# Kernel tuning notes

Measured on AMD Instinct MI355X. Metric: run time of the kernel, lower is better.

Reference implementation:

```python
import jax, jax.numpy as jnp
import numpy as np

WINDOW = 11
SIGMA = 1.5
CHANNELS = 3
C1 = 0.01 ** 2
C2 = 0.03 ** 2


def _gaussian_kernel(size=WINDOW, sigma=SIGMA, channels=CHANNELS):
    coords = jnp.arange(size, dtype=jnp.float32) - size // 2
    g = jnp.exp(-coords ** 2 / (2.0 * sigma ** 2))
    g = jnp.outer(g, g)
    g = g / g.sum()
    # depthwise kernel: [C, 1, K, K] (OIHW with feature_group_count=C)
    return jnp.broadcast_to(g[None, None], (channels, 1, size, size))


def _dwconv(x, kernel):
    # x: [N, C, H, W]; SAME padding, depthwise (groups = C)
    pad = WINDOW // 2
    return jax.lax.conv_general_dilated(
        x, kernel,
        window_strides=(1, 1),
        padding=[(pad, pad), (pad, pad)],
        dimension_numbers=('NCHW', 'OIHW', 'NCHW'),
        feature_group_count=CHANNELS,
    )


def setup_inputs() -> dict:
    key = jax.random.key(0)
    k1, k2 = jax.random.split(key)
    shape = (16, 3, 512, 512)
    pred = jax.random.uniform(k1, shape, dtype=jnp.float32)
    target = jax.random.uniform(k2, shape, dtype=jnp.float32)
    return {"pred": pred, "target": target}


def reference(pred, target):
    kernel = _gaussian_kernel().astype(pred.dtype)
    mu_p = _dwconv(pred, kernel)
    mu_t = _dwconv(target, kernel)
    mu_p2 = mu_p * mu_p
    mu_t2 = mu_t * mu_t
    mu_pt = mu_p * mu_t
    sigma_p2 = _dwconv(pred * pred, kernel) - mu_p2
    sigma_t2 = _dwconv(target * target, kernel) - mu_t2
    sigma_pt = _dwconv(pred * target, kernel) - mu_pt
    ssim_map = ((2.0 * mu_pt + C1) * (2.0 * sigma_pt + C2)) / (
        (mu_p2 + mu_t2 + C1) * (sigma_p2 + sigma_t2 + C2)
    )
    return 1.0 - ssim_map.mean()
```

## Files before the change

### kernel.cpp

```cpp
#include <hip/hip_runtime.h>
#include <math.h>

#define IMG_H 512
#define IMG_W 512
#define NSLOT 64
#define HT_R  56

typedef _Float16 f16x4 __attribute__((ext_vector_type(4)));
typedef _Float16 f16x8 __attribute__((ext_vector_type(8)));
typedef float    f32x4 __attribute__((ext_vector_type(4)));

__device__ __forceinline__ f16x8 pack8(const float4& a, const float4& b) {
    return f16x8{(_Float16)a.x, (_Float16)a.y, (_Float16)a.z, (_Float16)a.w,
                 (_Float16)b.x, (_Float16)b.y, (_Float16)b.z, (_Float16)b.w};
}

__device__ __forceinline__ f16x8 build_frag(int which, int l)
{
    const int lln = l & 15, llg = l >> 4;
    f16x8 f;
    #pragma unroll
    for (int j = 0; j < 8; ++j) {
        int idx = llg * 8 + j - lln - (which ? 0 : 3);
        float d = (float)(idx - 5);
        float v = 0.26601173f * exp2f(-d * d * 0.32059889f);
        f[j] = (_Float16)(((unsigned)idx <= 10u) ? v : 0.0f);
    }
    return f;
}

__global__ void ssim_frag_init(f16x8* __restrict__ frags)
{
    const int tid = threadIdx.x;
    if (tid < 128) frags[tid] = build_frag(tid >> 6, tid & 63);
}

__global__ __launch_bounds__(256, 6)
void ssim_main(const float* __restrict__ pred, const float* __restrict__ targ,
               const f16x8* __restrict__ frags, float* __restrict__ partial,
               double* __restrict__ acc, int mode)
{
    __shared__ _Float16 hT[2][5][16][HT_R];

    const int tid  = threadIdx.x;
    const int lane = tid & 63, wave = tid >> 6;
    const int ln   = lane & 15, lg = lane >> 4;
    const int ct   = wave >> 1, par = wave & 1;

    const int tx = blockIdx.x, ty = blockIdx.y, img = blockIdx.z;
    const float* __restrict__ p = pred + (size_t)img * (IMG_H * IMG_W);
    const float* __restrict__ t = targ + (size_t)img * (IMG_H * IMG_W);

    f16x8 Bw, A2w;
    if (frags) { Bw = frags[lane]; A2w = frags[64 + lane]; }
    else       { Bw = build_frag(0, lane); A2w = build_frag(1, lane); }

    const int rb0 = par ? 16 : 0;
    const int gc  = tx * 32 + ct * 16 + lg * 8 - 8;
    const bool colOK = (gc >= 0) && (gc <= IMG_W - 8);
    float4 P[2][2] = {}, T[2][2] = {};
    #pragma unroll
    for (int pos = 0; pos < 2; ++pos) {
        const int gr = ty * 32 - 5 + rb0 + 16 * pos + ln;
        if (colOK && gr >= 0 && gr < IMG_H) {
            const float* bp = p + (size_t)gr * IMG_W + gc;
            const float* bt = t + (size_t)gr * IMG_W + gc;
            P[pos][0] = ((const float4*)bp)[0];  P[pos][1] = ((const float4*)bp)[1];
            T[pos][0] = ((const float4*)bt)[0];  T[pos][1] = ((const float4*)bt)[1];
        }
    }
    const f32x4 z = {0.f, 0.f, 0.f, 0.f};

    #pragma unroll
    for (int pos = 0; pos < 2; ++pos) {
        const int rowbase = rb0 + 16 * pos;
        f16x8 pa = pack8(P[pos][0], P[pos][1]);
        f16x8 ta = pack8(T[pos][0], T[pos][1]);
        f16x8 fq[5];
        fq[0] = pa; fq[1] = ta;
        fq[2] = pa * pa; fq[3] = ta * ta; fq[4] = pa * ta;
        const int orow = rowbase + lg * 4;
        #pragma unroll
        for (int q = 0; q < 5; ++q) {
            f32x4 d = __builtin_amdgcn_mfma_f32_16x16x32_f16(fq[q], Bw, z, 0, 0, 0);
            *(f16x4*)&hT[ct][q][ln][orow] =
                f16x4{(_Float16)d[0], (_Float16)d[1], (_Float16)d[2], (_Float16)d[3]};
        }
    }

    float lsum = 0.f;
    {
        const int rbase = par * 16 + lg * 8;
        f32x4 accq[5];
        #pragma unroll
        for (int q = 0; q < 5; ++q) {
            f16x8 b = *(const f16x8*)&hT[ct][q][ln][rbase];
            accq[q] = __builtin_amdgcn_mfma_f32_16x16x32_f16(A2w, b, z, 0, 0, 0);
        }
        const float C1 = 1e-4f, C2 = 9e-4f;
        #pragma unroll
        for (int r = 0; r < 4; ++r) {
            float mp = accq[0][r], mt = accq[1][r];
            float vp = accq[2][r] - mp * mp;
            float vt = accq[3][r] - mt * mt;
            float cv = accq[4][r] - mp * mt;
            float num = (2.f * mp * mt + C1) * (2.f * cv + C2);
            float den = (mp * mp + mt * mt + C1) * (vp + vt + C2);
            lsum = fmaf(num, __builtin_amdgcn_rcpf(den), lsum);
        }
    }

    #pragma unroll
    for (int off = 32; off > 0; off >>= 1)
        lsum += __shfl_down(lsum, off, 64);
    if (lane == 0) {
        const int bid = (blockIdx.z * gridDim.y + blockIdx.y) * gridDim.x + blockIdx.x;
        if (mode == 0) partial[bid * 4 + wave] = lsum;
        else atomicAdd(&acc[(bid * 4 + wave) & (NSLOT - 1)], (double)lsum);
    }
}

__global__ void ssim_init(double* acc)
{
    if (threadIdx.x < NSLOT) acc[threadIdx.x] = 0.0;
}

__global__ __launch_bounds__(1024)
void ssim_fin_slots(const float* __restrict__ partial, float* __restrict__ out,
                    int n4, double inv_n)
{
    __shared__ double red[16];
    double s = 0.0;
    const int tid = threadIdx.x;
    for (int i = tid; i < n4; i += 1024) {
        float4 v = ((const float4*)partial)[i];
        s += (double)v.x + (double)v.y + (double)v.z + (double)v.w;
    }
    #pragma unroll
    for (int off = 32; off > 0; off >>= 1)
        s += __shfl_down(s, off, 64);
    if ((tid & 63) == 0) red[tid >> 6] = s;
    __syncthreads();
    if (tid == 0) {
        double tot = 0.0;
        #pragma unroll
        for (int w = 0; w < 16; ++w) tot += red[w];
        out[0] = (float)(1.0 - tot * inv_n);
    }
}

__global__ void ssim_fin_atomic(const double* __restrict__ acc, float* __restrict__ out,
                                double inv_n)
{
    if (threadIdx.x == 0) {
        double s = 0.0;
        for (int i = 0; i < NSLOT; ++i) s += acc[i];
        out[0] = (float)(1.0 - s * inv_n);
    }
}

extern "C" void kernel_launch(void* const* d_in, const int* in_sizes, int n_in,
                              void* d_out, int out_size, void* d_ws, size_t ws_size,
                              hipStream_t stream)
{
    const float* pred = (const float*)d_in[0];
    const float* targ = (const float*)d_in[1];
    float* out = (float*)d_out;

    const long long total = (long long)in_sizes[0];
    const int n_img = (int)(total / (IMG_H * IMG_W));
    dim3 grid(IMG_W / 32, IMG_H / 32, n_img);
    const int nblk = grid.x * grid.y * grid.z;
    const int nslots = nblk * 4;
    const double inv_n = 1.0 / (double)total;
    const size_t fragBytes = 128 * sizeof(f16x8);

    if (ws_size >= fragBytes + (size_t)nslots * sizeof(float)) {
        f16x8* frags   = (f16x8*)d_ws;
        float* partial = (float*)((char*)d_ws + fragBytes);
        hipLaunchKernelGGL(ssim_frag_init, dim3(1), dim3(128), 0, stream, frags);
        hipLaunchKernelGGL(ssim_main, grid, dim3(256), 0, stream,
                           pred, targ, (const f16x8*)frags, partial, (double*)nullptr, 0);
        hipLaunchKernelGGL(ssim_fin_slots, dim3(1), dim3(1024), 0, stream,
                           partial, out, nslots / 4, inv_n);
    } else {
        double* acc = (double*)d_ws;
        hipLaunchKernelGGL(ssim_init, dim3(1), dim3(64), 0, stream, acc);
        hipLaunchKernelGGL(ssim_main, grid, dim3(256), 0, stream,
                           pred, targ, (const f16x8*)nullptr, (float*)nullptr, acc, 1);
        hipLaunchKernelGGL(ssim_fin_atomic, dim3(1), dim3(1), 0, stream,
                           acc, out, inv_n);
    }
}
```

Before: 156.9 us.

## Fuse SSIM into one kernel with LDS-staged tiles and cross-image prefetch

Replaces the three-kernel pipeline (fragment init, main, final reduce) with a single fused kernel. Each block loads a 42x48 halo tile of pred and target into LDS once, so waves no longer refetch overlapping halo rows and columns, and it processes four images per block while prefetching the next image into registers. The final reduction uses a per-block double atomic plus a last-block counter, which removes the separate finish launch at the cost of a memset, atomic contention, and fewer blocks with more LDS barriers.

Result: slower. 262.8 us (+67.5%).

```diff
diff --git a/kernel.cpp b/kernel.cpp
--- a/kernel.cpp
+++ b/kernel.cpp
@@ -3,12 +3,20 @@
 
 #define IMG_H 512
 #define IMG_W 512
-#define NSLOT 64
-#define HT_R  56
+#define IPB   4
+#define SAB_S 56
+#define HT_S  56
 
 typedef _Float16 f16x4 __attribute__((ext_vector_type(4)));
 typedef _Float16 f16x8 __attribute__((ext_vector_type(8)));
 typedef float    f32x4 __attribute__((ext_vector_type(4)));
+
+__device__ __forceinline__ void lds_barrier() {
+    __asm__ volatile("" ::: "memory");
+    __builtin_amdgcn_s_waitcnt(0xC07F);
+    __builtin_amdgcn_s_barrier();
+    __asm__ volatile("" ::: "memory");
+}
 
 __device__ __forceinline__ f16x8 pack8(const float4& a, const float4& b) {
     return f16x8{(_Float16)a.x, (_Float16)a.y, (_Float16)a.z, (_Float16)a.w,
@@ -29,133 +37,151 @@
     return f;
 }
 
-__global__ void ssim_frag_init(f16x8* __restrict__ frags)
+__global__ __launch_bounds__(256, 4)
+void ssim_fused(const float* __restrict__ pred, const float* __restrict__ targ,
+                float* __restrict__ out, double* __restrict__ acc,
+                unsigned* __restrict__ counter, int n_img, int nblk, double inv_n)
 {
-    const int tid = threadIdx.x;
-    if (tid < 128) frags[tid] = build_frag(tid >> 6, tid & 63);
-}
-
-__global__ __launch_bounds__(256, 6)
-void ssim_main(const float* __restrict__ pred, const float* __restrict__ targ,
-               const f16x8* __restrict__ frags, float* __restrict__ partial,
-               double* __restrict__ acc, int mode)
-{
-    __shared__ _Float16 hT[2][5][16][HT_R];
+    __shared__ _Float16 sAB[2][48][SAB_S];
+    __shared__ _Float16 hT[5][32][HT_S];
+    __shared__ float red[4];
 
     const int tid  = threadIdx.x;
     const int lane = tid & 63, wave = tid >> 6;
     const int ln   = lane & 15, lg = lane >> 4;
-    const int ct   = wave >> 1, par = wave & 1;
-
-    const int tx = blockIdx.x, ty = blockIdx.y, img = blockIdx.z;
-    const float* __restrict__ p = pred + (size_t)img * (IMG_H * IMG_W);
-    const float* __restrict__ t = targ + (size_t)img * (IMG_H * IMG_W);
-
-    f16x8 Bw, A2w;
-    if (frags) { Bw = frags[lane]; A2w = frags[64 + lane]; }
-    else       { Bw = build_frag(0, lane); A2w = build_frag(1, lane); }
-
-    const int rb0 = par ? 16 : 0;
-    const int gc  = tx * 32 + ct * 16 + lg * 8 - 8;
-    const bool colOK = (gc >= 0) && (gc <= IMG_W - 8);
-    float4 P[2][2] = {}, T[2][2] = {};
+    const int tx = blockIdx.x, ty = blockIdx.y;
+
+    const int r0 = tid / 6,        g0 = tid % 6;
+    const bool has1 = (tid < 32);
+    const int r1 = (tid + 256) / 6, g1 = (tid + 256) % 6;
+
+    const int gr0 = ty * 32 - 5;
+    const int wo  = tx * 32 - 8;
+    auto valid = [&](int r, int g) {
+        int gr = gr0 + r;
+        return gr >= 0 && gr < IMG_H &&
+               !(tx == 0 && g == 0) && !(tx == 15 && g == 5);
+    };
+    const bool v0 = valid(r0, g0);
+    const bool v1 = has1 && valid(r1, g1);
+    const size_t off0 = (size_t)(gr0 + r0) * IMG_W + (wo + 8 * g0);
+    const size_t off1 = (size_t)(gr0 + r1) * IMG_W + (wo + 8 * g1);
+
+    const f16x8 Bw  = build_frag(0, lane);
+    const f16x8 A2w = build_frag(1, lane);
+    const f32x4 z = {0.f, 0.f, 0.f, 0.f};
+
+    const int imgBase = blockIdx.z * IPB;
+    float lsum = 0.f;
+
+    float4 P0a{0,0,0,0}, P0b{0,0,0,0}, T0a{0,0,0,0}, T0b{0,0,0,0};
+    float4 P1a{0,0,0,0}, P1b{0,0,0,0}, T1a{0,0,0,0}, T1b{0,0,0,0};
+    if (imgBase < n_img) {
+        const size_t ib = (size_t)imgBase * (IMG_H * IMG_W);
+        if (v0) {
+            const float* bp = pred + ib + off0; const float* bt = targ + ib + off0;
+            P0a = ((const float4*)bp)[0]; P0b = ((const float4*)bp)[1];
+            T0a = ((const float4*)bt)[0]; T0b = ((const float4*)bt)[1];
+        }
+        if (v1) {
+            const float* bp = pred + ib + off1; const float* bt = targ + ib + off1;
+            P1a = ((const float4*)bp)[0]; P1b = ((const float4*)bp)[1];
+            T1a = ((const float4*)bt)[0]; T1b = ((const float4*)bt)[1];
+        }
+    }
+
     #pragma unroll
-    for (int pos = 0; pos < 2; ++pos) {
-        const int gr = ty * 32 - 5 + rb0 + 16 * pos + ln;
-        if (colOK && gr >= 0 && gr < IMG_H) {
-            const float* bp = p + (size_t)gr * IMG_W + gc;
-            const float* bt = t + (size_t)gr * IMG_W + gc;
-            P[pos][0] = ((const float4*)bp)[0];  P[pos][1] = ((const float4*)bp)[1];
-            T[pos][0] = ((const float4*)bt)[0];  T[pos][1] = ((const float4*)bt)[1];
-        }
-    }
-    const f32x4 z = {0.f, 0.f, 0.f, 0.f};
-
-    #pragma unroll
-    for (int pos = 0; pos < 2; ++pos) {
-        const int rowbase = rb0 + 16 * pos;
-        f16x8 pa = pack8(P[pos][0], P[pos][1]);
-        f16x8 ta = pack8(T[pos][0], T[pos][1]);
-        f16x8 fq[5];
-        fq[0] = pa; fq[1] = ta;
-        fq[2] = pa * pa; fq[3] = ta * ta; fq[4] = pa * ta;
-        const int orow = rowbase + lg * 4;
-        #pragma unroll
-        for (int q = 0; q < 5; ++q) {
-            f32x4 d = __builtin_amdgcn_mfma_f32_16x16x32_f16(fq[q], Bw, z, 0, 0, 0);
-            *(f16x4*)&hT[ct][q][ln][orow] =
-                f16x4{(_Float16)d[0], (_Float16)d[1], (_Float16)d[2], (_Float16)d[3]};
-        }
-    }
-
-    float lsum = 0.f;
-    {
-        const int rbase = par * 16 + lg * 8;
-        f32x4 accq[5];
-        #pragma unroll
-        for (int q = 0; q < 5; ++q) {
-            f16x8 b = *(const f16x8*)&hT[ct][q][ln][rbase];
-            accq[q] = __builtin_amdgcn_mfma_f32_16x16x32_f16(A2w, b, z, 0, 0, 0);
-        }
-        const float C1 = 1e-4f, C2 = 9e-4f;
-        #pragma unroll
-        for (int r = 0; r < 4; ++r) {
-            float mp = accq[0][r], mt = accq[1][r];
-            float vp = accq[2][r] - mp * mp;
-            float vt = accq[3][r] - mt * mt;
-            float cv = accq[4][r] - mp * mt;
-            float num = (2.f * mp * mt + C1) * (2.f * cv + C2);
-            float den = (mp * mp + mt * mt + C1) * (vp + vt + C2);
-            lsum = fmaf(num, __builtin_amdgcn_rcpf(den), lsum);
+    for (int it = 0; it < IPB; ++it) {
+        const bool live = (imgBase + it < n_img);
+
+        *(f16x8*)&sAB[0][r0][8 * g0] = pack8(P0a, P0b);
+        *(f16x8*)&sAB[1][r0][8 * g0] = pack8(T0a, T0b);
+        if (has1) {
+            *(f16x8*)&sAB[0][r1][8 * g1] = pack8(P1a, P1b);
+            *(f16x8*)&sAB[1][r1][8 * g1] = pack8(T1a, T1b);
+        }
+
+        if (it + 1 < IPB) {
+            const int img2 = imgBase + it + 1;
+            P0a = {0,0,0,0}; P0b = {0,0,0,0}; T0a = {0,0,0,0}; T0b = {0,0,0,0};
+            P1a = {0,0,0,0}; P1b = {0,0,0,0}; T1a = {0,0,0,0}; T1b = {0,0,0,0};
+            if (img2 < n_img) {
+                const size_t ib = (size_t)img2 * (IMG_H * IMG_W);
+                if (v0) {
+                    const float* bp = pred + ib + off0; const float* bt = targ + ib + off0;
+                    P0a = ((const float4*)bp)[0]; P0b = ((const float4*)bp)[1];
+                    T0a = ((const float4*)bt)[0]; T0b = ((const float4*)bt)[1];
+                }
+                if (v1) {
+                    const float* bp = pred + ib + off1; const float* bt = targ + ib + off1;
+                    P1a = ((const float4*)bp)[0]; P1b = ((const float4*)bp)[1];
+                    T1a = ((const float4*)bt)[0]; T1b = ((const float4*)bt)[1];
+                }
+            }
+        }
+        lds_barrier();
+
+        auto do_tile = [&](int tt) {
+            const int rt = tt >> 1, ct = tt & 1;
+            const int rowbase = rt * 16;
+            f16x8 pa = *(const f16x8*)&sAB[0][rowbase + ln][ct * 16 + lg * 8];
+            f16x8 ta = *(const f16x8*)&sAB[1][rowbase + ln][ct * 16 + lg * 8];
+            f16x8 fq[5];
+            fq[0] = pa; fq[1] = ta;
+            fq[2] = pa * pa; fq[3] = ta * ta; fq[4] = pa * ta;
+            const int ocol = ct * 16 + ln;
+            const int orow = rowbase + lg * 4;
+            #pragma unroll
+            for (int q = 0; q < 5; ++q) {
+                f32x4 d = __builtin_amdgcn_mfma_f32_16x16x32_f16(fq[q], Bw, z, 0, 0, 0);
+                *(f16x4*)&hT[q][ocol][orow] =
+                    f16x4{(_Float16)d[0], (_Float16)d[1], (_Float16)d[2], (_Float16)d[3]};
+            }
+        };
+        do_tile(wave);
+        if (wave < 2) do_tile(wave + 4);
+        lds_barrier();
+
+        {
+            const int ctv = wave & 1, rtv = wave >> 1;
+            const int ocol  = ctv * 16 + ln;
+            const int rbase = rtv * 16 + lg * 8;
+            f32x4 accq[5];
+            #pragma unroll
+            for (int q = 0; q < 5; ++q) {
+                f16x8 b = *(const f16x8*)&hT[q][ocol][rbase];
+                accq[q] = __builtin_amdgcn_mfma_f32_16x16x32_f16(A2w, b, z, 0, 0, 0);
+            }
+            if (live) {
+                const float C1 = 1e-4f, C2 = 9e-4f;
+                #pragma unroll
+                for (int r = 0; r < 4; ++r) {
+                    float mp = accq[0][r], mt = accq[1][r];
+                    float vp = accq[2][r] - mp * mp;
+                    float vt = accq[3][r] - mt * mt;
+                    float cv = accq[4][r] - mp * mt;
+                    float num = (2.f * mp * mt + C1) * (2.f * cv + C2);
+                    float den = (mp * mp + mt * mt + C1) * (vp + vt + C2);
+                    lsum = fmaf(num, __builtin_amdgcn_rcpf(den), lsum);
+                }
+            }
         }
     }
 
     #pragma unroll
     for (int off = 32; off > 0; off >>= 1)
         lsum += __shfl_down(lsum, off, 64);
-    if (lane == 0) {
-        const int bid = (blockIdx.z * gridDim.y + blockIdx.y) * gridDim.x + blockIdx.x;
-        if (mode == 0) partial[bid * 4 + wave] = lsum;
-        else atomicAdd(&acc[(bid * 4 + wave) & (NSLOT - 1)], (double)lsum);
-    }
-}
-
-__global__ void ssim_init(double* acc)
-{
-    if (threadIdx.x < NSLOT) acc[threadIdx.x] = 0.0;
-}
-
-__global__ __launch_bounds__(1024)
-void ssim_fin_slots(const float* __restrict__ partial, float* __restrict__ out,
-                    int n4, double inv_n)
-{
-    __shared__ double red[16];
-    double s = 0.0;
-    const int tid = threadIdx.x;
-    for (int i = tid; i < n4; i += 1024) {
-        float4 v = ((const float4*)partial)[i];
-        s += (double)v.x + (double)v.y + (double)v.z + (double)v.w;
-    }
-    #pragma unroll
-    for (int off = 32; off > 0; off >>= 1)
-        s += __shfl_down(s, off, 64);
-    if ((tid & 63) == 0) red[tid >> 6] = s;
+    if (lane == 0) red[wave] = lsum;
     __syncthreads();
     if (tid == 0) {
-        double tot = 0.0;
-        #pragma unroll
-        for (int w = 0; w < 16; ++w) tot += red[w];
-        out[0] = (float)(1.0 - tot * inv_n);
-    }
-}
-
-__global__ void ssim_fin_atomic(const double* __restrict__ acc, float* __restrict__ out,
-                                double inv_n)
-{
-    if (threadIdx.x == 0) {
-        double s = 0.0;
-        for (int i = 0; i < NSLOT; ++i) s += acc[i];
-        out[0] = (float)(1.0 - s * inv_n);
+        double bs = (double)red[0] + (double)red[1] + (double)red[2] + (double)red[3];
+        atomicAdd(acc, bs);
+        __threadfence();
+        unsigned old = atomicAdd(counter, 1u);
+        if (old == (unsigned)(nblk - 1)) {
+            double tot = atomicAdd(acc, 0.0);
+            out[0] = (float)(1.0 - tot * inv_n);
+        }
     }
 }
 
@@ -169,26 +195,15 @@
 
     const long long total = (long long)in_sizes[0];
     const int n_img = (int)(total / (IMG_H * IMG_W));
-    dim3 grid(IMG_W / 32, IMG_H / 32, n_img);
+    const int nz = (n_img + IPB - 1) / IPB;
+    dim3 grid(IMG_W / 32, IMG_H / 32, nz);
     const int nblk = grid.x * grid.y * grid.z;
-    const int nslots = nblk * 4;
     const double inv_n = 1.0 / (double)total;
-    const size_t fragBytes = 128 * sizeof(f16x8);
-
-    if (ws_size >= fragBytes + (size_t)nslots * sizeof(float)) {
-        f16x8* frags   = (f16x8*)d_ws;
-        float* partial = (float*)((char*)d_ws + fragBytes);
-        hipLaunchKernelGGL(ssim_frag_init, dim3(1), dim3(128), 0, stream, frags);
-        hipLaunchKernelGGL(ssim_main, grid, dim3(256), 0, stream,
-                           pred, targ, (const f16x8*)frags, partial, (double*)nullptr, 0);
-        hipLaunchKernelGGL(ssim_fin_slots, dim3(1), dim3(1024), 0, stream,
-                           partial, out, nslots / 4, inv_n);
-    } else {
-        double* acc = (double*)d_ws;
-        hipLaunchKernelGGL(ssim_init, dim3(1), dim3(64), 0, stream, acc);
-        hipLaunchKernelGGL(ssim_main, grid, dim3(256), 0, stream,
-                           pred, targ, (const f16x8*)nullptr, (float*)nullptr, acc, 1);
-        hipLaunchKernelGGL(ssim_fin_atomic, dim3(1), dim3(1), 0, stream,
-                           acc, out, inv_n);
-    }
-}
+
+    double*   acc     = (double*)d_ws;
+    unsigned* counter = (unsigned*)((char*)d_ws + 8);
+
+    hipMemsetAsync(d_ws, 0, 16, stream);
+    hipLaunchKernelGGL(ssim_fused, grid, dim3(256), 0, stream,
+                       pred, targ, out, acc, counter, n_img, nblk, inv_n);
+}
```
